# Optimization experiments

Hardware: AMD Instinct MI355X
Metric: run time of the kernel (lower is better)

The kernel has to match this reference:

```python
import jax, jax.numpy as jnp
import numpy as np

B, H, N = 16, 12, 784

def setup_inputs() -> dict:
    key = jax.random.key(0)
    mha_masks = jax.random.uniform(key, (B, H, N, N), dtype=jnp.float32)
    return {"mha_masks": mha_masks}

def reference(mha_masks) -> jnp.ndarray:
    # Original loop builds cross_attn[b,i,j,l] = m[b,i,j]*m[b,i,l] and sums over j,
    # which equals m[b,i,l] * rowsum_j m[b,i,j]. Compute that directly (O(B*H*N^2)).
    b, h, n, _ = mha_masks.shape
    rowsum = mha_masks.sum(axis=-1, keepdims=True)          # [B,H,N,1]
    aggregated = (mha_masks * rowsum).sum(axis=1)           # sum over heads -> [B,N,N]
    # softmax over the flattened N*N per batch element
    meta = jax.nn.softmax(aggregated.reshape(b, -1), axis=1).reshape(b, n, n)
    return meta
```

## Files before the change

### kernel.cpp

```cpp
#include <hip/hip_runtime.h>

#define B_ 16
#define H_ 12
#define N_ 784
#define NN_ (N_ * N_)
#define NF4_ (N_ / 4)
#define BPB_ 128

__global__ void init_kernel(int* __restrict__ maxbits, float* __restrict__ sums) {
    int t = threadIdx.x;
    if (t < B_) { maxbits[t] = 0; sums[t] = 0.0f; }
}

__global__ __launch_bounds__(256) void agg_kernel(
    const float* __restrict__ m, float* __restrict__ agg,
    int* __restrict__ maxbits) {
    const int lane = threadIdx.x & 63;
    const int wave = threadIdx.x >> 6;
    const int row  = blockIdx.x * 4 + wave;
    const int b = row / N_;
    const int i = row - b * N_;

    float4 acc[4];
#pragma unroll
    for (int k = 0; k < 4; ++k) acc[k] = make_float4(0.f, 0.f, 0.f, 0.f);

#pragma unroll
    for (int h = 0; h < H_; ++h) {
        const float4* p =
            (const float4*)m + ((size_t)(b * H_ + h) * N_ + i) * NF4_;
        float4 r[4];
        float s = 0.f;
#pragma unroll
        for (int k = 0; k < 4; ++k) {
            int idx = k * 64 + lane;
            if (idx < NF4_) {
                r[k] = p[idx];
                s += r[k].x + r[k].y + r[k].z + r[k].w;
            } else {
                r[k] = make_float4(0.f, 0.f, 0.f, 0.f);
            }
        }
#pragma unroll
        for (int off = 32; off > 0; off >>= 1) s += __shfl_xor(s, off, 64);
#pragma unroll
        for (int k = 0; k < 4; ++k) {
            acc[k].x += r[k].x * s;
            acc[k].y += r[k].y * s;
            acc[k].z += r[k].z * s;
            acc[k].w += r[k].w * s;
        }
    }

    float4* outp = (float4*)agg + ((size_t)b * N_ + i) * NF4_;
    float mx = 0.f;
#pragma unroll
    for (int k = 0; k < 4; ++k) {
        int idx = k * 64 + lane;
        if (idx < NF4_) {
            outp[idx] = acc[k];
            mx = fmaxf(mx, fmaxf(fmaxf(acc[k].x, acc[k].y),
                                 fmaxf(acc[k].z, acc[k].w)));
        }
    }
#pragma unroll
    for (int off = 32; off > 0; off >>= 1)
        mx = fmaxf(mx, __shfl_xor(mx, off, 64));
    if (lane == 0) atomicMax(&maxbits[b], __float_as_int(mx));
}

__global__ __launch_bounds__(256) void expsum_kernel(
    float* __restrict__ agg, const int* __restrict__ maxbits,
    float* __restrict__ sums) {
    const int b   = blockIdx.x / BPB_;
    const int blk = blockIdx.x % BPB_;
    const float mx = __int_as_float(maxbits[b]);
    float4* p = (float4*)agg + (size_t)b * (NN_ / 4);
    float s = 0.f;
    for (int idx = blk * 256 + threadIdx.x; idx < NN_ / 4; idx += BPB_ * 256) {
        float4 v = p[idx];
        v.x = __expf(v.x - mx);
        v.y = __expf(v.y - mx);
        v.z = __expf(v.z - mx);
        v.w = __expf(v.w - mx);
        p[idx] = v;
        s += v.x + v.y + v.z + v.w;
    }
#pragma unroll
    for (int off = 32; off > 0; off >>= 1) s += __shfl_xor(s, off, 64);
    __shared__ float red[4];
    if ((threadIdx.x & 63) == 0) red[threadIdx.x >> 6] = s;
    __syncthreads();
    if (threadIdx.x == 0)
        atomicAdd(&sums[b], red[0] + red[1] + red[2] + red[3]);
}

__global__ __launch_bounds__(256) void scale_kernel(
    float* __restrict__ agg, const float* __restrict__ sums) {
    const int b   = blockIdx.x / BPB_;
    const int blk = blockIdx.x % BPB_;
    const float inv = 1.0f / sums[b];
    float4* p = (float4*)agg + (size_t)b * (NN_ / 4);
    for (int idx = blk * 256 + threadIdx.x; idx < NN_ / 4; idx += BPB_ * 256) {
        float4 v = p[idx];
        v.x *= inv; v.y *= inv; v.z *= inv; v.w *= inv;
        p[idx] = v;
    }
}

extern "C" void kernel_launch(void* const* d_in, const int* in_sizes, int n_in,
                              void* d_out, int out_size, void* d_ws,
                              size_t ws_size, hipStream_t stream) {
    const float* m = (const float*)d_in[0];
    float* out = (float*)d_out;
    int*   maxbits = (int*)d_ws;
    float* sums    = (float*)((char*)d_ws + B_ * sizeof(int));

    hipLaunchKernelGGL(init_kernel, dim3(1), dim3(64), 0, stream,
                       maxbits, sums);
    hipLaunchKernelGGL(agg_kernel, dim3(B_ * N_ / 4), dim3(256), 0, stream,
                       m, out, maxbits);
    hipLaunchKernelGGL(expsum_kernel, dim3(B_ * BPB_), dim3(256), 0, stream,
                       out, maxbits, sums);
    hipLaunchKernelGGL(scale_kernel, dim3(B_ * BPB_), dim3(256), 0, stream,
                       out, sums);
}
```

Baseline: 724.4 us.

## Fuse online softmax stats into aggregation and merge exp with scaling pass

The aggregation kernel now computes a per-row max and exp-sum with an online-softmax combine and writes them to a small stats buffer. This replaces the atomic max and the separate init kernel. A single finalize kernel reduces each batch's row stats and applies exp and normalisation in one read-modify-write pass. That removes one full read+write sweep over the output and two launches, at the cost of extra exp work in the aggregation epilogue and every finalize block redundantly reducing 784 stats.

Result: faster. 627.9 us (-13.3%).

```diff
diff --git a/kernel.cpp b/kernel.cpp
--- a/kernel.cpp
+++ b/kernel.cpp
@@ -7,103 +7,109 @@
 #define NF4_ (N_ / 4)
 #define BPB_ 128
 
-__global__ void init_kernel(int* __restrict__ maxbits, float* __restrict__ sums) {
-    int t = threadIdx.x;
-    if (t < B_) { maxbits[t] = 0; sums[t] = 0.0f; }
-}
 
-__global__ __launch_bounds__(256) void agg_kernel(
+__global__ __launch_bounds__(256) void agg_stats_kernel(
     const float* __restrict__ m, float* __restrict__ agg,
-    int* __restrict__ maxbits) {
+    float2* __restrict__ stats) {
     const int lane = threadIdx.x & 63;
     const int wave = threadIdx.x >> 6;
     const int row  = blockIdx.x * 4 + wave;
     const int b = row / N_;
     const int i = row - b * N_;
 
-    float4 acc[4];
-#pragma unroll
-    for (int k = 0; k < 4; ++k) acc[k] = make_float4(0.f, 0.f, 0.f, 0.f);
+    float4 a0 = make_float4(0.f, 0.f, 0.f, 0.f);
+    float4 a1 = a0, a2 = a0, a3 = a0;
 
-#pragma unroll
+#pragma unroll 2
     for (int h = 0; h < H_; ++h) {
         const float4* p =
             (const float4*)m + ((size_t)(b * H_ + h) * N_ + i) * NF4_;
-        float4 r[4];
-        float s = 0.f;
-#pragma unroll
-        for (int k = 0; k < 4; ++k) {
-            int idx = k * 64 + lane;
-            if (idx < NF4_) {
-                r[k] = p[idx];
-                s += r[k].x + r[k].y + r[k].z + r[k].w;
-            } else {
-                r[k] = make_float4(0.f, 0.f, 0.f, 0.f);
-            }
-        }
+        float4 r0 = p[lane];
+        float4 r1 = p[lane + 64];
+        float4 r2 = p[lane + 128];
+        float4 r3 = (lane < NF4_ - 192) ? p[lane + 192]
+                                        : make_float4(0.f, 0.f, 0.f, 0.f);
+        float s = ((r0.x + r0.y) + (r0.z + r0.w))
+                + ((r1.x + r1.y) + (r1.z + r1.w))
+                + ((r2.x + r2.y) + (r2.z + r2.w))
+                + ((r3.x + r3.y) + (r3.z + r3.w));
 #pragma unroll
         for (int off = 32; off > 0; off >>= 1) s += __shfl_xor(s, off, 64);
-#pragma unroll
-        for (int k = 0; k < 4; ++k) {
-            acc[k].x += r[k].x * s;
-            acc[k].y += r[k].y * s;
-            acc[k].z += r[k].z * s;
-            acc[k].w += r[k].w * s;
-        }
+        a0.x += r0.x * s; a0.y += r0.y * s; a0.z += r0.z * s; a0.w += r0.w * s;
+        a1.x += r1.x * s; a1.y += r1.y * s; a1.z += r1.z * s; a1.w += r1.w * s;
+        a2.x += r2.x * s; a2.y += r2.y * s; a2.z += r2.z * s; a2.w += r2.w * s;
+        a3.x += r3.x * s; a3.y += r3.y * s; a3.z += r3.z * s; a3.w += r3.w * s;
     }
 
     float4* outp = (float4*)agg + ((size_t)b * N_ + i) * NF4_;
-    float mx = 0.f;
+    outp[lane]       = a0;
+    outp[lane + 64]  = a1;
+    outp[lane + 128] = a2;
+    if (lane < NF4_ - 192) outp[lane + 192] = a3;
+
+    float mx = fmaxf(fmaxf(fmaxf(a0.x, a0.y), fmaxf(a0.z, a0.w)),
+                     fmaxf(fmaxf(a1.x, a1.y), fmaxf(a1.z, a1.w)));
+    mx = fmaxf(mx, fmaxf(fmaxf(a2.x, a2.y), fmaxf(a2.z, a2.w)));
+    if (lane < NF4_ - 192)
+        mx = fmaxf(mx, fmaxf(fmaxf(a3.x, a3.y), fmaxf(a3.z, a3.w)));
+
+    float es = __expf(a0.x - mx) + __expf(a0.y - mx)
+             + __expf(a0.z - mx) + __expf(a0.w - mx)
+             + __expf(a1.x - mx) + __expf(a1.y - mx)
+             + __expf(a1.z - mx) + __expf(a1.w - mx)
+             + __expf(a2.x - mx) + __expf(a2.y - mx)
+             + __expf(a2.z - mx) + __expf(a2.w - mx);
+    if (lane < NF4_ - 192)
+        es += __expf(a3.x - mx) + __expf(a3.y - mx)
+            + __expf(a3.z - mx) + __expf(a3.w - mx);
+
 #pragma unroll
-    for (int k = 0; k < 4; ++k) {
-        int idx = k * 64 + lane;
-        if (idx < NF4_) {
-            outp[idx] = acc[k];
-            mx = fmaxf(mx, fmaxf(fmaxf(acc[k].x, acc[k].y),
-                                 fmaxf(acc[k].z, acc[k].w)));
-        }
+    for (int off = 32; off > 0; off >>= 1) {
+        float om = __shfl_xor(mx, off, 64);
+        float os = __shfl_xor(es, off, 64);
+        float nm = fmaxf(mx, om);
+        es = es * __expf(mx - nm) + os * __expf(om - nm);
+        mx = nm;
+    }
+    if (lane == 0) stats[row] = make_float2(mx, es);
+}
+
+__global__ __launch_bounds__(256) void finalize_kernel(
+    float* __restrict__ agg, const float2* __restrict__ stats) {
+    const int b   = blockIdx.x / BPB_;
+    const int blk = blockIdx.x % BPB_;
+
+    float mR = 0.f, sR = 0.f;
+    for (int r = threadIdx.x; r < N_; r += 256) {
+        float2 t = stats[b * N_ + r];
+        float nm = fmaxf(mR, t.x);
+        sR = sR * __expf(mR - nm) + t.y * __expf(t.x - nm);
+        mR = nm;
     }
 #pragma unroll
-    for (int off = 32; off > 0; off >>= 1)
-        mx = fmaxf(mx, __shfl_xor(mx, off, 64));
-    if (lane == 0) atomicMax(&maxbits[b], __float_as_int(mx));
-}
+    for (int off = 32; off > 0; off >>= 1) {
+        float om = __shfl_xor(mR, off, 64);
+        float os = __shfl_xor(sR, off, 64);
+        float nm = fmaxf(mR, om);
+        sR = sR * __expf(mR - nm) + os * __expf(om - nm);
+        mR = nm;
+    }
+    __shared__ float2 red[4];
+    if ((threadIdx.x & 63) == 0) red[threadIdx.x >> 6] = make_float2(mR, sR);
+    __syncthreads();
+    float2 p0 = red[0], p1 = red[1], p2 = red[2], p3 = red[3];
+    const float gm = fmaxf(fmaxf(p0.x, p1.x), fmaxf(p2.x, p3.x));
+    const float S  = p0.y * __expf(p0.x - gm) + p1.y * __expf(p1.x - gm)
+                   + p2.y * __expf(p2.x - gm) + p3.y * __expf(p3.x - gm);
+    const float inv = 1.0f / S;
 
-__global__ __launch_bounds__(256) void expsum_kernel(
-    float* __restrict__ agg, const int* __restrict__ maxbits,
-    float* __restrict__ sums) {
-    const int b   = blockIdx.x / BPB_;
-    const int blk = blockIdx.x % BPB_;
-    const float mx = __int_as_float(maxbits[b]);
-    float4* p = (float4*)agg + (size_t)b * (NN_ / 4);
-    float s = 0.f;
-    for (int idx = blk * 256 + threadIdx.x; idx < NN_ / 4; idx += BPB_ * 256) {
-        float4 v = p[idx];
-        v.x = __expf(v.x - mx);
-        v.y = __expf(v.y - mx);
-        v.z = __expf(v.z - mx);
-        v.w = __expf(v.w - mx);
-        p[idx] = v;
-        s += v.x + v.y + v.z + v.w;
-    }
-#pragma unroll
-    for (int off = 32; off > 0; off >>= 1) s += __shfl_xor(s, off, 64);
-    __shared__ float red[4];
-    if ((threadIdx.x & 63) == 0) red[threadIdx.x >> 6] = s;
-    __syncthreads();
-    if (threadIdx.x == 0)
-        atomicAdd(&sums[b], red[0] + red[1] + red[2] + red[3]);
-}
-
-__global__ __launch_bounds__(256) void scale_kernel(
-    float* __restrict__ agg, const float* __restrict__ sums) {
-    const int b   = blockIdx.x / BPB_;
-    const int blk = blockIdx.x % BPB_;
-    const float inv = 1.0f / sums[b];
     float4* p = (float4*)agg + (size_t)b * (NN_ / 4);
     for (int idx = blk * 256 + threadIdx.x; idx < NN_ / 4; idx += BPB_ * 256) {
         float4 v = p[idx];
-        v.x *= inv; v.y *= inv; v.z *= inv; v.w *= inv;
+        v.x = __expf(v.x - gm) * inv;
+        v.y = __expf(v.y - gm) * inv;
+        v.z = __expf(v.z - gm) * inv;
+        v.w = __expf(v.w - gm) * inv;
         p[idx] = v;
     }
 }
@@ -113,15 +119,10 @@
                               size_t ws_size, hipStream_t stream) {
     const float* m = (const float*)d_in[0];
     float* out = (float*)d_out;
-    int*   maxbits = (int*)d_ws;
-    float* sums    = (float*)((char*)d_ws + B_ * sizeof(int));
+    float2* stats = (float2*)d_ws;
 
-    hipLaunchKernelGGL(init_kernel, dim3(1), dim3(64), 0, stream,
-                       maxbits, sums);
-    hipLaunchKernelGGL(agg_kernel, dim3(B_ * N_ / 4), dim3(256), 0, stream,
-                       m, out, maxbits);
-    hipLaunchKernelGGL(expsum_kernel, dim3(B_ * BPB_), dim3(256), 0, stream,
-                       out, maxbits, sums);
-    hipLaunchKernelGGL(scale_kernel, dim3(B_ * BPB_), dim3(256), 0, stream,
-                       out, sums);
+    hipLaunchKernelGGL(agg_stats_kernel, dim3(B_ * N_ / 4), dim3(256), 0,
+                       stream, m, out, stats);
+    hipLaunchKernelGGL(finalize_kernel, dim3(B_ * BPB_), dim3(256), 0,
+                       stream, out, stats);
 }
```
